# Performance work log

Hardware: AMD Instinct MI355X
Metric: run time of the kernel (lower is better)

Reference implementation:

```python
import jax, jax.numpy as jnp
import numpy as np

PAD = 0

def setup_inputs() -> dict:
    key = jax.random.key(0)
    ks = jax.random.split(key, 16)
    B, S, D, F = 64, 512, 768, 256
    VOCAB = 32000
    # variable-length tweets: length in [8, S], rest is padding (token id PAD=0)
    lengths = jax.random.randint(ks[0], (B,), 8, S + 1)
    tok = jax.random.randint(ks[1], (B, S), 1, VOCAB)
    x = jnp.where(jnp.arange(S)[None, :] < lengths[:, None], tok, PAD)
    h = jax.random.normal(ks[2], (B, S, D), dtype=jnp.float32)
    sc = 0.02
    w2 = jax.random.normal(ks[3], (F, D, 2), dtype=jnp.float32) * sc
    b2 = jax.random.normal(ks[4], (F,), dtype=jnp.float32) * sc
    w3 = jax.random.normal(ks[5], (F, D, 3), dtype=jnp.float32) * sc
    b3 = jax.random.normal(ks[6], (F,), dtype=jnp.float32) * sc
    w4 = jax.random.normal(ks[7], (F, D, 4), dtype=jnp.float32) * sc
    b4 = jax.random.normal(ks[8], (F,), dtype=jnp.float32) * sc
    w5 = jax.random.normal(ks[9], (F, D, 5), dtype=jnp.float32) * sc
    b5 = jax.random.normal(ks[10], (F,), dtype=jnp.float32) * sc
    fc_w = jax.random.normal(ks[11], (1, 4 * F), dtype=jnp.float32) * sc
    fc_b = jax.random.normal(ks[12], (1,), dtype=jnp.float32) * sc
    return {"x": x, "h": h, "w2": w2, "b2": b2, "w3": w3, "b3": b3,
            "w4": w4, "b4": b4, "w5": w5, "b5": b5, "fc_w": fc_w, "fc_b": fc_b}


def _branch(hc, L, w, b):
    # hc: [B, D, S] front-compacted hidden states; w: [F, D, k]
    k = w.shape[-1]
    out = jax.lax.conv_general_dilated(
        hc, w, window_strides=(1,), padding='VALID',
        dimension_numbers=('NCH', 'OIH', 'NCH')) + b[None, :, None]  # [B,F,S-k+1]
    T = out.shape[-1]
    # conv position t is valid iff t + k - 1 < L  <=>  t < L - k + 1
    valid = jnp.arange(T)[None, :] < (L - k + 1)[:, None]           # [B,T]
    neg = jnp.asarray(-jnp.inf, out.dtype)
    pooled = jnp.max(jnp.where(valid[:, None, :], out, neg), axis=-1)  # [B,F]
    return jax.nn.relu(pooled)


def reference(x, h, w2, b2, w3, b3, w4, b4, w5, b5, fc_w, fc_b):
    mask = x != PAD                                   # [B,S]
    L = mask.sum(axis=1)                              # [B]
    # stable compaction: move non-pad token hidden states to the front, order preserved
    order = jnp.argsort(jnp.logical_not(mask), axis=1, stable=True)   # [B,S]
    hc = jnp.take_along_axis(h, order[..., None], axis=1)             # [B,S,D]
    hc = hc.transpose(0, 2, 1)                                        # [B,D,S]
    feats = jnp.concatenate([
        _branch(hc, L, w2, b2),
        _branch(hc, L, w3, b3),
        _branch(hc, L, w4, b4),
        _branch(hc, L, w5, b5),
    ], axis=-1)                                       # [B, 4F]
    logits = feats @ fc_w.T + fc_b                    # [B,1]
    return jax.nn.sigmoid(logits).squeeze(-1)         # [B]
```

## Files before the change

kernel.cpp:

```cpp
#include <hip/hip_runtime.h>
#include <stdint.h>

#define Bn 64
#define Sn 512
#define SPn 520
#define Dn 768
#define JSTRIDE 196608
#define ABUF 8448
#define BSLOT 8192
#define QS_A 28.222222f
#define SAQ 0.035433072f

typedef int iv4 __attribute__((ext_vector_type(4)));

static __device__ __forceinline__ signed char q8(float f, float s) {
  float t = __builtin_rintf(f * s);
  t = fmaxf(-127.f, fminf(127.f, t));
  return (signed char)(int)t;
}

static __device__ __forceinline__ void gload16(const void* g, void* l) {
  __builtin_amdgcn_global_load_lds(
      (const __attribute__((address_space(1))) unsigned int*)g,
      (__attribute__((address_space(3))) unsigned int*)l, 16, 0, 0);
}

template<int N> __device__ __forceinline__ void waitv() {
  static_assert(N == 0 || N == 2 || N == 5, "");
  if constexpr (N == 0) asm volatile("s_waitcnt vmcnt(0)" ::: "memory");
  else if constexpr (N == 2) asm volatile("s_waitcnt vmcnt(2)" ::: "memory");
  else asm volatile("s_waitcnt vmcnt(5)" ::: "memory");
}

__global__ __launch_bounds__(256) void plan_kernel(
    const int* __restrict__ x, int* __restrict__ plan, int* __restrict__ rowmap,
    int* __restrict__ feats) {
  __shared__ int sL[64];
  __shared__ int sOff[65];
  int tid = threadIdx.x, lane = tid & 63, wv = tid >> 6;
  {
    int4 z = {0, 0, 0, 0};
    for (int i = tid * 4; i < 65536; i += 1024) *(int4*)(feats + i) = z;
  }
  for (int bb = wv; bb < 64; bb += 4) {
    int cnt = 0;
    for (int c = 0; c < 8; ++c) {
      unsigned long long m = __ballot(x[bb * Sn + c * 64 + lane] != 0);
      cnt += __popcll(m);
    }
    if (lane == 0) sL[bb] = cnt;
  }
  __syncthreads();
  if (tid < 64) {
    int L = sL[tid];
    int SL = (L + 15) & ~15;
    int pre = SL;
    #pragma unroll
    for (int off = 1; off < 64; off <<= 1) {
      int y = __shfl_up(pre, off);
      if (tid >= off) pre += y;
    }
    sOff[tid] = pre - SL;
    if (tid == 63) { sOff[64] = pre; plan[0] = (pre + 127) >> 7; }
  }
  __syncthreads();
  int M = sOff[64];
  for (int b = 0; b < 64; ++b) {
    int off = sOff[b], L = sL[b];
    int SL = (L + 15) & ~15;
    int enc = (b << 20) | (L << 10);
    for (int t = tid; t < SL; t += 256) rowmap[off + t] = enc | t;
  }
  for (int p = M + tid; p < M + 264; p += 256)
    rowmap[p] = 512;
}

__global__ __launch_bounds__(256) void stage_kernel(
    const int* __restrict__ x, const float* __restrict__ h,
    const float* __restrict__ w2, const float* __restrict__ w3,
    const float* __restrict__ w4, const float* __restrict__ w5,
    signed char* __restrict__ hcq, signed char* __restrict__ wq,
    float* __restrict__ fscale) {
  int tid = threadIdx.x, lane = tid & 63, wv = tid >> 6;
  if (blockIdx.x < 512) {
    int cidx = blockIdx.x;
    int b = cidx >> 3, rblk = cidx & 7;
    __shared__ unsigned long long masks[8];
    __shared__ short sidx[Sn];
    for (int c = wv; c < 8; c += 4) {
      unsigned long long m = __ballot(x[b * Sn + c * 64 + lane] != 0);
      if (lane == 0) masks[c] = m;
    }
    __syncthreads();
    int pref[9]; pref[0] = 0;
    #pragma unroll
    for (int c = 0; c < 8; ++c) pref[c + 1] = pref[c] + __popcll(masks[c]);
    int L = pref[8];
    for (int p = tid; p < Sn; p += 256) {
      int c = p >> 6, l = p & 63;
      unsigned long long m = masks[c];
      if ((m >> l) & 1ull)
        sidx[pref[c] + __popcll(m & ((1ull << l) - 1ull))] = (short)p;
    }
    __syncthreads();
    int r0 = rblk * 65;
    for (int r = r0 + wv; r < r0 + 65; r += 4) {
      if (r < L) {
        signed char* dst = hcq + ((size_t)b * SPn + r) * Dn;
        const float* src = h + ((size_t)b * Sn + sidx[r]) * Dn;
        #pragma unroll
        for (int c = 0; c < 3; ++c) {
          int d = c * 256 + lane * 4;
          float4 v = *(const float4*)(src + d);
          char4 o = { q8(v.x, QS_A), q8(v.y, QS_A), q8(v.z, QS_A), q8(v.w, QS_A) };
          *(char4*)(dst + d) = o;
        }
      }
    }
  } else {
    __shared__ float sf[3840];
    __shared__ float smax[4];
    int bb = blockIdx.x - 512;
    int br = bb >> 8, f = bb & 255, k = br + 2;
    const float* w = (br == 0) ? w2 : (br == 1) ? w3 : (br == 2) ? w4 : w5;
    int mBase = 256 * ((br * (br + 3)) >> 1);
    const float* src = w + (size_t)f * Dn * k;
    int n = Dn * k;
    float mx = 0.f;
    for (int e = tid; e < n; e += 256) {
      float v = src[e];
      sf[e] = v;
      mx = fmaxf(mx, fabsf(v));
    }
    #pragma unroll
    for (int off = 32; off; off >>= 1) mx = fmaxf(mx, __shfl_xor(mx, off));
    if (lane == 0) smax[wv] = mx;
    __syncthreads();
    float M = fmaxf(fmaxf(smax[0], smax[1]), fmaxf(smax[2], smax[3]));
    M = fmaxf(M, 1e-30f);
    if (tid == 0) fscale[br * 256 + f] = M / 127.f;
    float qs = 127.f / M;
    for (int j = 0; j < k; ++j) {
      signed char* dst = wq + (size_t)(mBase + j * 256 + f) * Dn;
      for (int d4 = tid * 4; d4 < Dn; d4 += 1024) {
        char4 o = { q8(sf[(d4 + 0) * k + j], qs), q8(sf[(d4 + 1) * k + j], qs),
                    q8(sf[(d4 + 2) * k + j], qs), q8(sf[(d4 + 3) * k + j], qs) };
        *(char4*)(dst + d4) = o;
      }
    }
  }
}

static __device__ __forceinline__ void issueA(
    int d0i, char* sA, const char* const (&gA)[2], const char* gAt,
    int lane, int wvoff) {
  int aoff = (d0i + 1) * 64;
  char* nA = sA + ((d0i + 1) & 1) * ABUF;
  gload16(gA[0] + aoff, nA + wvoff);
  gload16(gA[1] + aoff, nA + 4096 + wvoff);
  if (lane < 16) gload16(gAt + aoff, nA + 8192);
}

template<int J, int W, int J2, int DADD, int DOA>
static __device__ __forceinline__ void conv_step(
    int d0i, int bsl0, char* sA, char* sB,
    const char* const (&gA)[2], const char* gAt, const char* gB0,
    int lane, int wr, int wc, int lrow, int lg, int wvoff, iv4 (&acc)[4][4]) {
  int sl = bsl0 + J;      sl  -= (sl  >= 3) ? 3 : 0; sl  -= (sl  >= 3) ? 3 : 0;
  int dsl = bsl0 + J + 2; dsl -= (dsl >= 3) ? 3 : 0; dsl -= (dsl >= 3) ? 3 : 0;
  {
    int boff = J2 * JSTRIDE + (d0i + DADD) * 64;
    char* bdst = sB + dsl * BSLOT + wvoff;
    gload16(gB0 + boff, bdst);
    gload16(gB0 + 49152 + boff, bdst + 4096);
  }
  if constexpr (DOA) issueA(d0i, sA, gA, gAt, lane, wvoff);
  const char* curA = sA + (d0i & 1) * ABUF;
  const char* curB = sB + sl * BSLOT;
  iv4 Af[4], Bf[4];
  #pragma unroll
  for (int m = 0; m < 4; ++m) {
    int row = wr * 64 + m * 16 + lrow + J;
    Af[m] = *(const iv4*)(curA + row * 64 + ((lg ^ ((row >> 1) & 3)) << 4));
  }
  #pragma unroll
  for (int n = 0; n < 4; ++n) {
    int row = wc * 64 + n * 16 + lrow;
    Bf[n] = *(const iv4*)(curB + row * 64 + ((lg ^ ((row >> 1) & 3)) << 4));
  }
  __builtin_amdgcn_s_setprio(1);
  #pragma unroll
  for (int n = 0; n < 4; ++n)
    #pragma unroll
    for (int m = 0; m < 4; ++m)
      acc[m][n] = __builtin_amdgcn_mfma_i32_16x16x64_i8(Af[m], Bf[n], acc[m][n], 0, 0, 0);
  __builtin_amdgcn_s_setprio(0);
  __builtin_amdgcn_sched_barrier(0);
  waitv<W>();
  __builtin_amdgcn_sched_barrier(0);
  __builtin_amdgcn_s_barrier();
  __builtin_amdgcn_sched_barrier(0);
}

#define SA bsl0, sA, sB, gA, gAt, gB0, lane, wr, wc, lrow, lg, wvoff, acc

template<int KK>
static __device__ __forceinline__ void conv_loop(
    char* sA, char* sB, const char* const (&gA)[2], const char* gAt,
    const char* gB0,
    int lane, int wr, int wc, int lrow, int lg, int wvoff, iv4 (&acc)[4][4]) {
  gload16(gA[0], sA + wvoff);
  gload16(gA[1], sA + 4096 + wvoff);
  if (lane < 16) gload16(gAt, sA + 8192);
  gload16(gB0, sB + wvoff);
  gload16(gB0 + 49152, sB + 4096 + wvoff);
  gload16(gB0 + JSTRIDE, sB + BSLOT + wvoff);
  gload16(gB0 + 49152 + JSTRIDE, sB + BSLOT + 4096 + wvoff);
  __builtin_amdgcn_sched_barrier(0);
  waitv<2>();
  __builtin_amdgcn_sched_barrier(0);
  __builtin_amdgcn_s_barrier();
  __builtin_amdgcn_sched_barrier(0);
  int bsl0 = 0;
  for (int d0i = 0; d0i < 11; ++d0i) {
    if constexpr (KK == 5) {
      conv_step<0,5,2,0,1>(d0i, SA);
      conv_step<1,5,3,0,0>(d0i, SA);
      conv_step<2,2,4,0,0>(d0i, SA);
      conv_step<3,2,0,1,0>(d0i, SA);
      conv_step<4,2,1,1,0>(d0i, SA);
    } else if constexpr (KK == 4) {
      conv_step<0,5,2,0,1>(d0i, SA);
      conv_step<1,5,3,0,0>(d0i, SA);
      conv_step<2,2,0,1,0>(d0i, SA);
      conv_step<3,2,1,1,0>(d0i, SA);
    } else if constexpr (KK == 3) {
      conv_step<0,5,2,0,1>(d0i, SA);
      conv_step<1,5,0,1,0>(d0i, SA);
      conv_step<2,2,1,1,0>(d0i, SA);
    } else {
      conv_step<0,5,0,1,1>(d0i, SA);
      conv_step<1,2,1,1,0>(d0i, SA);
    }
    bsl0 += KK; bsl0 -= (bsl0 >= 3) ? 3 : 0; bsl0 -= (bsl0 >= 3) ? 3 : 0;
  }
  if constexpr (KK == 5) {
    conv_step<0,2,2,0,0>(11, SA);
    conv_step<1,2,3,0,0>(11, SA);
    conv_step<2,2,4,0,0>(11, SA);
    conv_step<3,2,0,1,0>(11, SA);
    conv_step<4,2,1,1,0>(11, SA);
  } else if constexpr (KK == 4) {
    conv_step<0,2,2,0,0>(11, SA);
    conv_step<1,2,3,0,0>(11, SA);
    conv_step<2,2,0,1,0>(11, SA);
    conv_step<3,2,1,1,0>(11, SA);
  } else if constexpr (KK == 3) {
    conv_step<0,2,2,0,0>(11, SA);
    conv_step<1,2,0,1,0>(11, SA);
    conv_step<2,2,1,1,0>(11, SA);
  } else {
    conv_step<0,2,0,1,0>(11, SA);
    conv_step<1,2,1,1,0>(11, SA);
  }
  waitv<0>();
}

__global__ __launch_bounds__(256, 3) void conv_kernel(
    const signed char* __restrict__ hcq, const signed char* __restrict__ wq,
    const float* __restrict__ b2, const float* __restrict__ b3,
    const float* __restrict__ b4, const float* __restrict__ b5,
    const float* __restrict__ fscale,
    const int* __restrict__ plan, const int* __restrict__ rowmap,
    int* __restrict__ feats) {
  __shared__ char smem[2 * ABUF + 3 * BSLOT];
  char* sA = smem;
  char* sB = smem + 2 * ABUF;
  int idx = blockIdx.x;
  int xcd = idx & 7, s2 = idx >> 3;
  int sub = s2 & 7, tile = xcd + ((s2 >> 3) << 3);
  if (tile >= plan[0]) return;
  int br = 3 - (sub >> 1), ff = sub & 1, kk = br + 2;
  int mBase = 256 * ((br * (br + 3)) >> 1) + ff * 128;
  const float* bias = (br == 0) ? b2 : (br == 1) ? b3 : (br == 2) ? b4 : b5;
  int tid = threadIdx.x, lane = tid & 63, wv = tid >> 6;
  int wr = wv >> 1, wc = wv & 1;
  int lrow = lane & 15, lg = lane >> 4;
  int wvoff = wv * 1024;
  int P0 = tile << 7;

  const char* gA[2];
  #pragma unroll
  for (int p = 0; p < 2; ++p) {
    int c = p * 256 + tid;
    int row = c >> 2, sgp = c & 3;
    int rm = rowmap[P0 + row];
    int bb_ = rm >> 20, t = rm & 1023;
    int seg = sgp ^ ((row >> 1) & 3);
    gA[p] = (const char*)(hcq + ((size_t)(bb_ * SPn + t)) * Dn + seg * 16);
  }
  const char* gAt;
  {
    int l = lane & 15;
    int row = 128 + (l >> 2), sgp = l & 3;
    int rm = rowmap[P0 + row];
    int bb_ = rm >> 20, t = rm & 1023;
    int seg = sgp ^ ((row >> 1) & 3);
    gAt = (const char*)(hcq + ((size_t)(bb_ * SPn + t)) * Dn + seg * 16);
  }
  const char* gB0;
  {
    int row = tid >> 2, sgp = tid & 3;
    int seg = sgp ^ ((row >> 1) & 3);
    gB0 = (const char*)(wq + ((size_t)(mBase + row)) * Dn + seg * 16);
  }

  iv4 acc[4][4];
  #pragma unroll
  for (int m = 0; m < 4; ++m)
    #pragma unroll
    for (int n = 0; n < 4; ++n) acc[m][n] = (iv4)0;

  switch (br) {
    case 3: conv_loop<5>(sA, sB, gA, gAt, gB0, lane, wr, wc, lrow, lg, wvoff, acc); break;
    case 2: conv_loop<4>(sA, sB, gA, gAt, gB0, lane, wr, wc, lrow, lg, wvoff, acc); break;
    case 1: conv_loop<3>(sA, sB, gA, gAt, gB0, lane, wr, wc, lrow, lg, wvoff, acc); break;
    default: conv_loop<2>(sA, sB, gA, gAt, gB0, lane, wr, wc, lrow, lg, wvoff, acc); break;
  }

  int rmv[4];
  #pragma unroll
  for (int m = 0; m < 4; ++m) rmv[m] = rowmap[P0 + wr * 64 + m * 16];
  #pragma unroll
  for (int n = 0; n < 4; ++n) {
    int fg = ff * 128 + wc * 64 + n * 16 + lrow;
    float bv = bias[fg];
    float sfc = fscale[br * 256 + fg] * SAQ;
    #pragma unroll
    for (int m = 0; m < 4; ++m) {
      int bb_ = rmv[m] >> 20;
      int Lb = (rmv[m] >> 10) & 1023;
      int t0 = (rmv[m] & 1023) + lg * 4;
      int vlim = Lb - kk + 1;
      float pmax = 0.f;
      #pragma unroll
      for (int i = 0; i < 4; ++i) {
        float v = (float)acc[m][n][i] * sfc + bv;
        pmax = fmaxf(pmax, (t0 + i < vlim) ? fmaxf(v, 0.f) : 0.f);
      }
      pmax = fmaxf(pmax, __shfl_xor(pmax, 16));
      pmax = fmaxf(pmax, __shfl_xor(pmax, 32));
      if (lane < 16 && pmax > 0.f)
        atomicMax(feats + bb_ * 1024 + br * 256 + fg, __float_as_int(pmax));
    }
  }
}

__global__ __launch_bounds__(64) void fc_kernel(
    const int* __restrict__ feats, const float* __restrict__ fcw,
    const float* __restrict__ fcb, float* __restrict__ out) {
  int b = blockIdx.x, lane = threadIdx.x;
  float acc = 0.f;
  for (int i = lane; i < 1024; i += 64)
    acc += __int_as_float(feats[b * 1024 + i]) * fcw[i];
  #pragma unroll
  for (int off = 32; off; off >>= 1) acc += __shfl_xor(acc, off);
  if (lane == 0) out[b] = 1.f / (1.f + expf(-(acc + fcb[0])));
}

extern "C" void kernel_launch(void* const* d_in, const int* in_sizes, int n_in,
                              void* d_out, int out_size, void* d_ws, size_t ws_size,
                              hipStream_t stream) {
  const int*   x   = (const int*)d_in[0];
  const float* h   = (const float*)d_in[1];
  const float* w2  = (const float*)d_in[2];
  const float* b2  = (const float*)d_in[3];
  const float* w3  = (const float*)d_in[4];
  const float* b3  = (const float*)d_in[5];
  const float* w4  = (const float*)d_in[6];
  const float* b4  = (const float*)d_in[7];
  const float* w5  = (const float*)d_in[8];
  const float* b5  = (const float*)d_in[9];
  const float* fcw = (const float*)d_in[10];
  const float* fcb = (const float*)d_in[11];
  float* out = (float*)d_out;
  char* ws = (char*)d_ws;
  signed char* hcq = (signed char*)ws;
  signed char* wq  = (signed char*)(ws + 25559040);
  float* fscale = (float*)(ws + 28311552);
  int* feats  = (int*)(ws + 28315648);
  int* plan   = (int*)(ws + 28577792);
  int* rowmap = (int*)(ws + 28577808);

  plan_kernel<<<1, 256, 0, stream>>>(x, plan, rowmap, feats);
  stage_kernel<<<1536, 256, 0, stream>>>(x, h, w2, w3, w4, w5, hcq, wq, fscale);
  conv_kernel<<<2048, 256, 0, stream>>>(hcq, wq, b2, b3, b4, b5, fscale, plan, rowmap, feats);
  fc_kernel<<<64, 64, 0, stream>>>(feats, fcw, fcb, out);
}
```

Before: 112.4 us.

## Load conv weights directly into registers instead of staging through LDS

Weight (B) fragments are now read from global memory straight into registers, with the next tap's fragment loaded one step ahead, instead of being staged through a triple-buffered LDS ring. The wave layout changes from a 2x2 grid to 4 waves each owning 32 filters across all 128 rows (8x2 accumulators). This removes the per-tap LDS round trip and most block barriers, leaving only one barrier per D-chunk for the A buffer. In exchange the A tile is read from LDS twice as often per wave, and register-held weight loads may expose global latency that the previous async LDS pipeline hid.

Result: slower. 126.6 us (+12.7%).

```diff
diff --git a/kernel.cpp b/kernel.cpp
--- a/kernel.cpp
+++ b/kernel.cpp
@@ -7,7 +7,6 @@
 #define Dn 768
 #define JSTRIDE 196608
 #define ABUF 8448
-#define BSLOT 8192
 #define QS_A 28.222222f
 #define SAQ 0.035433072f
 
@@ -25,11 +24,9 @@
       (__attribute__((address_space(3))) unsigned int*)l, 16, 0, 0);
 }
 
-template<int N> __device__ __forceinline__ void waitv() {
-  static_assert(N == 0 || N == 2 || N == 5, "");
-  if constexpr (N == 0) asm volatile("s_waitcnt vmcnt(0)" ::: "memory");
-  else if constexpr (N == 2) asm volatile("s_waitcnt vmcnt(2)" ::: "memory");
-  else asm volatile("s_waitcnt vmcnt(5)" ::: "memory");
+template<int S, typename T, int N>
+static __device__ __forceinline__ T (&sel(T (&a)[N], T (&b)[N]))[N] {
+  if constexpr (S) return b; else return a;
 }
 
 __global__ __launch_bounds__(256) void plan_kernel(
@@ -161,109 +158,71 @@
   if (lane < 16) gload16(gAt + aoff, nA + 8192);
 }
 
-template<int J, int W, int J2, int DADD, int DOA>
-static __device__ __forceinline__ void conv_step(
-    int d0i, int bsl0, char* sA, char* sB,
-    const char* const (&gA)[2], const char* gAt, const char* gB0,
-    int lane, int wr, int wc, int lrow, int lg, int wvoff, iv4 (&acc)[4][4]) {
-  int sl = bsl0 + J;      sl  -= (sl  >= 3) ? 3 : 0; sl  -= (sl  >= 3) ? 3 : 0;
-  int dsl = bsl0 + J + 2; dsl -= (dsl >= 3) ? 3 : 0; dsl -= (dsl >= 3) ? 3 : 0;
-  {
-    int boff = J2 * JSTRIDE + (d0i + DADD) * 64;
-    char* bdst = sB + dsl * BSLOT + wvoff;
-    gload16(gB0 + boff, bdst);
-    gload16(gB0 + 49152 + boff, bdst + 4096);
-  }
+template<int KK, int J, int PH, int LAST>
+static __device__ __forceinline__ void jstep(
+    int d0i, const char* curA, const char* const (&gB)[2],
+    int lrow, int lg, iv4 (&Ba)[2], iv4 (&Bb)[2], iv4 (&acc)[8][2]) {
+  if constexpr (!LAST || J + 1 < KK) {
+    constexpr int tap = (J + 1) % KK;
+    constexpr int da  = (J + 1) / KK;
+    iv4 (&Bpre)[2] = sel<(PH + J + 1) & 1>(Ba, Bb);
+    int off = tap * JSTRIDE + (d0i + da) * 64;
+    Bpre[0] = *(const iv4*)(gB[0] + off);
+    Bpre[1] = *(const iv4*)(gB[1] + off);
+  }
+  iv4 Af[8];
+  #pragma unroll
+  for (int m = 0; m < 8; ++m) {
+    int row = m * 16 + lrow + J;
+    Af[m] = *(const iv4*)(curA + row * 64 + ((lg ^ ((row >> 1) & 3)) << 4));
+  }
+  iv4 (&Bc)[2] = sel<(PH + J) & 1>(Ba, Bb);
+  #pragma unroll
+  for (int m = 0; m < 8; ++m) {
+    acc[m][0] = __builtin_amdgcn_mfma_i32_16x16x64_i8(Af[m], Bc[0], acc[m][0], 0, 0, 0);
+    acc[m][1] = __builtin_amdgcn_mfma_i32_16x16x64_i8(Af[m], Bc[1], acc[m][1], 0, 0, 0);
+  }
+}
+
+template<int KK, int PH, int LAST, int DOA>
+static __device__ __forceinline__ void d0_body(
+    int d0i, char* sA, const char* const (&gA)[2], const char* gAt,
+    const char* const (&gB)[2], int lane, int lrow, int lg, int wvoff,
+    iv4 (&Ba)[2], iv4 (&Bb)[2], iv4 (&acc)[8][2]) {
   if constexpr (DOA) issueA(d0i, sA, gA, gAt, lane, wvoff);
   const char* curA = sA + (d0i & 1) * ABUF;
-  const char* curB = sB + sl * BSLOT;
-  iv4 Af[4], Bf[4];
-  #pragma unroll
-  for (int m = 0; m < 4; ++m) {
-    int row = wr * 64 + m * 16 + lrow + J;
-    Af[m] = *(const iv4*)(curA + row * 64 + ((lg ^ ((row >> 1) & 3)) << 4));
-  }
-  #pragma unroll
-  for (int n = 0; n < 4; ++n) {
-    int row = wc * 64 + n * 16 + lrow;
-    Bf[n] = *(const iv4*)(curB + row * 64 + ((lg ^ ((row >> 1) & 3)) << 4));
-  }
-  __builtin_amdgcn_s_setprio(1);
-  #pragma unroll
-  for (int n = 0; n < 4; ++n)
-    #pragma unroll
-    for (int m = 0; m < 4; ++m)
-      acc[m][n] = __builtin_amdgcn_mfma_i32_16x16x64_i8(Af[m], Bf[n], acc[m][n], 0, 0, 0);
-  __builtin_amdgcn_s_setprio(0);
-  __builtin_amdgcn_sched_barrier(0);
-  waitv<W>();
-  __builtin_amdgcn_sched_barrier(0);
-  __builtin_amdgcn_s_barrier();
-  __builtin_amdgcn_sched_barrier(0);
-}
-
-#define SA bsl0, sA, sB, gA, gAt, gB0, lane, wr, wc, lrow, lg, wvoff, acc
+  jstep<KK,0,PH,LAST>(d0i, curA, gB, lrow, lg, Ba, Bb, acc);
+  if constexpr (KK > 1) jstep<KK,1,PH,LAST>(d0i, curA, gB, lrow, lg, Ba, Bb, acc);
+  if constexpr (KK > 2) jstep<KK,2,PH,LAST>(d0i, curA, gB, lrow, lg, Ba, Bb, acc);
+  if constexpr (KK > 3) jstep<KK,3,PH,LAST>(d0i, curA, gB, lrow, lg, Ba, Bb, acc);
+  if constexpr (KK > 4) jstep<KK,4,PH,LAST>(d0i, curA, gB, lrow, lg, Ba, Bb, acc);
+  if constexpr (!LAST) __syncthreads();
+}
 
 template<int KK>
 static __device__ __forceinline__ void conv_loop(
-    char* sA, char* sB, const char* const (&gA)[2], const char* gAt,
-    const char* gB0,
-    int lane, int wr, int wc, int lrow, int lg, int wvoff, iv4 (&acc)[4][4]) {
+    char* sA, const char* const (&gA)[2], const char* gAt,
+    const char* const (&gB)[2], int lane, int lrow, int lg, int wvoff,
+    iv4 (&acc)[8][2]) {
+  iv4 Ba[2], Bb[2];
   gload16(gA[0], sA + wvoff);
   gload16(gA[1], sA + 4096 + wvoff);
   if (lane < 16) gload16(gAt, sA + 8192);
-  gload16(gB0, sB + wvoff);
-  gload16(gB0 + 49152, sB + 4096 + wvoff);
-  gload16(gB0 + JSTRIDE, sB + BSLOT + wvoff);
-  gload16(gB0 + 49152 + JSTRIDE, sB + BSLOT + 4096 + wvoff);
-  __builtin_amdgcn_sched_barrier(0);
-  waitv<2>();
-  __builtin_amdgcn_sched_barrier(0);
-  __builtin_amdgcn_s_barrier();
-  __builtin_amdgcn_sched_barrier(0);
-  int bsl0 = 0;
-  for (int d0i = 0; d0i < 11; ++d0i) {
-    if constexpr (KK == 5) {
-      conv_step<0,5,2,0,1>(d0i, SA);
-      conv_step<1,5,3,0,0>(d0i, SA);
-      conv_step<2,2,4,0,0>(d0i, SA);
-      conv_step<3,2,0,1,0>(d0i, SA);
-      conv_step<4,2,1,1,0>(d0i, SA);
-    } else if constexpr (KK == 4) {
-      conv_step<0,5,2,0,1>(d0i, SA);
-      conv_step<1,5,3,0,0>(d0i, SA);
-      conv_step<2,2,0,1,0>(d0i, SA);
-      conv_step<3,2,1,1,0>(d0i, SA);
-    } else if constexpr (KK == 3) {
-      conv_step<0,5,2,0,1>(d0i, SA);
-      conv_step<1,5,0,1,0>(d0i, SA);
-      conv_step<2,2,1,1,0>(d0i, SA);
-    } else {
-      conv_step<0,5,0,1,1>(d0i, SA);
-      conv_step<1,2,1,1,0>(d0i, SA);
-    }
-    bsl0 += KK; bsl0 -= (bsl0 >= 3) ? 3 : 0; bsl0 -= (bsl0 >= 3) ? 3 : 0;
-  }
-  if constexpr (KK == 5) {
-    conv_step<0,2,2,0,0>(11, SA);
-    conv_step<1,2,3,0,0>(11, SA);
-    conv_step<2,2,4,0,0>(11, SA);
-    conv_step<3,2,0,1,0>(11, SA);
-    conv_step<4,2,1,1,0>(11, SA);
-  } else if constexpr (KK == 4) {
-    conv_step<0,2,2,0,0>(11, SA);
-    conv_step<1,2,3,0,0>(11, SA);
-    conv_step<2,2,0,1,0>(11, SA);
-    conv_step<3,2,1,1,0>(11, SA);
-  } else if constexpr (KK == 3) {
-    conv_step<0,2,2,0,0>(11, SA);
-    conv_step<1,2,0,1,0>(11, SA);
-    conv_step<2,2,1,1,0>(11, SA);
+  Ba[0] = *(const iv4*)(gB[0]);
+  Ba[1] = *(const iv4*)(gB[1]);
+  __syncthreads();
+  if constexpr ((KK & 1) == 0) {
+    for (int d0i = 0; d0i < 11; ++d0i)
+      d0_body<KK,0,0,1>(d0i, sA, gA, gAt, gB, lane, lrow, lg, wvoff, Ba, Bb, acc);
+    d0_body<KK,0,1,0>(11, sA, gA, gAt, gB, lane, lrow, lg, wvoff, Ba, Bb, acc);
   } else {
-    conv_step<0,2,0,1,0>(11, SA);
-    conv_step<1,2,1,1,0>(11, SA);
-  }
-  waitv<0>();
+    for (int dd = 0; dd < 5; ++dd) {
+      d0_body<KK,0,0,1>(2 * dd,     sA, gA, gAt, gB, lane, lrow, lg, wvoff, Ba, Bb, acc);
+      d0_body<KK,1,0,1>(2 * dd + 1, sA, gA, gAt, gB, lane, lrow, lg, wvoff, Ba, Bb, acc);
+    }
+    d0_body<KK,0,0,1>(10, sA, gA, gAt, gB, lane, lrow, lg, wvoff, Ba, Bb, acc);
+    d0_body<KK,1,1,0>(11, sA, gA, gAt, gB, lane, lrow, lg, wvoff, Ba, Bb, acc);
+  }
 }
 
 __global__ __launch_bounds__(256, 3) void conv_kernel(
@@ -273,9 +232,8 @@
     const float* __restrict__ fscale,
     const int* __restrict__ plan, const int* __restrict__ rowmap,
     int* __restrict__ feats) {
-  __shared__ char smem[2 * ABUF + 3 * BSLOT];
+  __shared__ char smem[2 * ABUF];
   char* sA = smem;
-  char* sB = smem + 2 * ABUF;
   int idx = blockIdx.x;
   int xcd = idx & 7, s2 = idx >> 3;
   int sub = s2 & 7, tile = xcd + ((s2 >> 3) << 3);
@@ -284,7 +242,7 @@
   int mBase = 256 * ((br * (br + 3)) >> 1) + ff * 128;
   const float* bias = (br == 0) ? b2 : (br == 1) ? b3 : (br == 2) ? b4 : b5;
   int tid = threadIdx.x, lane = tid & 63, wv = tid >> 6;
-  int wr = wv >> 1, wc = wv & 1;
+  int wc = wv;
   int lrow = lane & 15, lg = lane >> 4;
   int wvoff = wv * 1024;
   int P0 = tile << 7;
@@ -308,36 +266,36 @@
     int seg = sgp ^ ((row >> 1) & 3);
     gAt = (const char*)(hcq + ((size_t)(bb_ * SPn + t)) * Dn + seg * 16);
   }
-  const char* gB0;
-  {
-    int row = tid >> 2, sgp = tid & 3;
-    int seg = sgp ^ ((row >> 1) & 3);
-    gB0 = (const char*)(wq + ((size_t)(mBase + row)) * Dn + seg * 16);
-  }
-
-  iv4 acc[4][4];
-  #pragma unroll
-  for (int m = 0; m < 4; ++m)
-    #pragma unroll
-    for (int n = 0; n < 4; ++n) acc[m][n] = (iv4)0;
+  const char* gB[2];
+  #pragma unroll
+  for (int n = 0; n < 2; ++n) {
+    int row = wc * 32 + n * 16 + lrow;
+    gB[n] = (const char*)(wq + (size_t)(mBase + row) * Dn + lg * 16);
+  }
+
+  iv4 acc[8][2];
+  #pragma unroll
+  for (int m = 0; m < 8; ++m) {
+    acc[m][0] = (iv4)0; acc[m][1] = (iv4)0;
+  }
 
   switch (br) {
-    case 3: conv_loop<5>(sA, sB, gA, gAt, gB0, lane, wr, wc, lrow, lg, wvoff, acc); break;
-    case 2: conv_loop<4>(sA, sB, gA, gAt, gB0, lane, wr, wc, lrow, lg, wvoff, acc); break;
-    case 1: conv_loop<3>(sA, sB, gA, gAt, gB0, lane, wr, wc, lrow, lg, wvoff, acc); break;
-    default: conv_loop<2>(sA, sB, gA, gAt, gB0, lane, wr, wc, lrow, lg, wvoff, acc); break;
-  }
-
-  int rmv[4];
-  #pragma unroll
-  for (int m = 0; m < 4; ++m) rmv[m] = rowmap[P0 + wr * 64 + m * 16];
-  #pragma unroll
-  for (int n = 0; n < 4; ++n) {
-    int fg = ff * 128 + wc * 64 + n * 16 + lrow;
+    case 3: conv_loop<5>(sA, gA, gAt, gB, lane, lrow, lg, wvoff, acc); break;
+    case 2: conv_loop<4>(sA, gA, gAt, gB, lane, lrow, lg, wvoff, acc); break;
+    case 1: conv_loop<3>(sA, gA, gAt, gB, lane, lrow, lg, wvoff, acc); break;
+    default: conv_loop<2>(sA, gA, gAt, gB, lane, lrow, lg, wvoff, acc); break;
+  }
+
+  int rmv[8];
+  #pragma unroll
+  for (int m = 0; m < 8; ++m) rmv[m] = rowmap[P0 + m * 16];
+  #pragma unroll
+  for (int n = 0; n < 2; ++n) {
+    int fg = ff * 128 + wc * 32 + n * 16 + lrow;
     float bv = bias[fg];
     float sfc = fscale[br * 256 + fg] * SAQ;
     #pragma unroll
-    for (int m = 0; m < 4; ++m) {
+    for (int m = 0; m < 8; ++m) {
       int bb_ = rmv[m] >> 20;
       int Lb = (rmv[m] >> 10) & 1023;
       int t0 = (rmv[m] & 1023) + lg * 4;
```
